# Optimization experiments

Measured on AMD Instinct MI355X. Metric: run time of the kernel, lower is better.

The kernel has to match this reference:

```python
import jax, jax.numpy as jnp
import numpy as np

D = 768          # emb_dim (BERT hidden size)
N_DOM = 9        # domain_num
N_EXP = 6        # num_expert (per-domain)
N_SH = 4         # num_shared_expert
N_TOT = N_EXP + N_SH  # total experts seen by the gate
B = 2048


def _p(key, shape, scale=0.02):
    return jax.random.normal(key, shape, dtype=jnp.float32) * scale


def setup_inputs() -> dict:
    key = jax.random.key(0)
    ks = jax.random.split(key, 32)
    inp = {
        "content_pooled": jax.random.normal(ks[0], (B, D), dtype=jnp.float32),
        "ftr_pooled": jax.random.normal(ks[1], (B, D), dtype=jnp.float32),
        "category": jax.random.randint(ks[2], (B,), 0, N_DOM, dtype=jnp.int64),
        "domain_emb": _p(ks[3], (N_DOM, D), 1.0),
    }
    # per-domain expert stacks: Linear(D,D)-SiLU-Linear(D,D), for content (c) and ftr (f)
    for pre, base in (("c", 4), ("f", 12)):
        inp[pre + "W1"] = _p(ks[base + 0], (N_DOM, N_EXP, D, D))
        inp[pre + "b1"] = jnp.zeros((N_DOM, N_EXP, D), jnp.float32)
        inp[pre + "W2"] = _p(ks[base + 1], (N_DOM, N_EXP, D, D))
        inp[pre + "b2"] = jnp.zeros((N_DOM, N_EXP, D), jnp.float32)
        # shared experts: Linear(D,D)-SiLU-Linear(D,D)
        inp[pre + "sW1"] = _p(ks[base + 2], (N_SH, D, D))
        inp[pre + "sb1"] = jnp.zeros((N_SH, D), jnp.float32)
        inp[pre + "sW2"] = _p(ks[base + 3], (N_SH, D, D))
        inp[pre + "sb2"] = jnp.zeros((N_SH, D), jnp.float32)
        # per-domain enhanced gates: Linear(2D,D)-SiLU-Linear(D,N_TOT), temperature scalar per domain
        inp[pre + "gW1"] = _p(ks[base + 4], (N_DOM, 2 * D, D))
        inp[pre + "gb1"] = jnp.zeros((N_DOM, D), jnp.float32)
        inp[pre + "gW2"] = _p(ks[base + 5], (N_DOM, D, N_TOT))
        inp[pre + "gb2"] = jnp.zeros((N_DOM, N_TOT), jnp.float32)
        inp[pre + "temp"] = jnp.ones((N_DOM,), jnp.float32)
    return inp


def _moe_branch(x, category, domain_emb, W1, b1, W2, b2,
                sW1, sb1, sW2, sb2, gW1, gb1, gW2, gb2, temp):
    # x: [B, D]; category: [B] int in [0, N_DOM)
    demb = domain_emb[category]                           # [B, D]
    g_in = jnp.concatenate([demb, x], axis=-1)            # [B, 2D]
    # gate computed for all domains, then per-example domain selected
    gh = jax.nn.silu(jnp.einsum("bx,nxh->bnh", g_in, gW1) + gb1)      # [B, 9, D]
    logits = jnp.einsum("bnh,nhe->bne", gh, gW2) + gb2                 # [B, 9, 10]
    t = jax.nn.softplus(temp) + 1e-4                                    # positive temperature
    gates_all = jax.nn.softmax(logits / t[None, :, None], axis=-1)
    gates = jnp.take_along_axis(gates_all, category[:, None, None], axis=1)[:, 0]  # [B, 10]
    # per-domain experts for all domains (grouped GEMM form), then select domain
    h1 = jax.nn.silu(jnp.einsum("bd,nedh->bneh", x, W1) + b1)          # [B, 9, 6, D]
    e_all = jnp.einsum("bneh,nehd->bned", h1, W2) + b2                 # [B, 9, 6, D]
    e_dom = jnp.take_along_axis(e_all, category[:, None, None, None], axis=1)[:, 0]  # [B, 6, D]
    # shared experts
    hs = jax.nn.silu(jnp.einsum("bd,edh->beh", x, sW1) + sb1)          # [B, 4, D]
    e_sh = jnp.einsum("beh,ehd->bed", hs, sW2) + sb2                   # [B, 4, D]
    experts = jnp.concatenate([e_dom, e_sh], axis=1)                   # [B, 10, D]
    return jnp.einsum("be,bed->bd", gates, experts)                    # [B, D]


def reference(content_pooled, ftr_pooled, category, domain_emb,
              cW1, cb1, cW2, cb2, csW1, csb1, csW2, csb2,
              cgW1, cgb1, cgW2, cgb2, ctemp,
              fW1, fb1, fW2, fb2, fsW1, fsb1, fsW2, fsb2,
              fgW1, fgb1, fgW2, fgb2, ftemp):
    c_out = _moe_branch(content_pooled, category, domain_emb,
                        cW1, cb1, cW2, cb2, csW1, csb1, csW2, csb2,
                        cgW1, cgb1, cgW2, cgb2, ctemp)
    f_out = _moe_branch(ftr_pooled, category, domain_emb,
                        fW1, fb1, fW2, fb2, fsW1, fsb1, fsW2, fsb2,
                        fgW1, fgb1, fgW2, fgb2, ftemp)
    return jnp.concatenate([c_out, f_out], axis=-1)  # [B, 2D]
```

## Files before the change

kernel.cpp:

```cpp
#include <hip/hip_runtime.h>

#define D_ 768
#define B_ 2048
#define NDOM 9
#define NTOT 10
#define MT 128
#define NT 128
#define KT 32
#define KI1 (D_ / KT)

#define E2   589824ull
#define E2G  1179648ull
#define OFF_WT2 31850496ull
#define OFF_SW1 63700992ull
#define OFF_SW2 66060288ull
#define OFF_GW1 68419584ull
#define ZWE     79036416ull

typedef _Float16 f16;
typedef _Float16 f16x8 __attribute__((ext_vector_type(8)));
typedef _Float16 f16x2 __attribute__((ext_vector_type(2)));
typedef float f32x4 __attribute__((ext_vector_type(4)));

typedef const __attribute__((address_space(1))) void gas_void;
typedef __attribute__((address_space(3))) void las_void;

__device__ __forceinline__ void gload16(const f16* g, f16* l) {
  __builtin_amdgcn_global_load_lds((gas_void*)g, (las_void*)l, 16, 0, 0);
}

#define WAITV4() asm volatile("s_waitcnt vmcnt(4)" ::: "memory")
#define WAITV0() asm volatile("s_waitcnt vmcnt(0)" ::: "memory")
#define SBAR()   do { __builtin_amdgcn_s_barrier(); __builtin_amdgcn_sched_barrier(0); } while (0)

__global__ __launch_bounds__(256) void bucket_kernel(const int* cat32, int* perm,
                                                     int* off, int* cnt, int* dom) {
  __shared__ int scnt[NDOM], soff[NDOM], scur[NDOM];
  __shared__ int odd_nz;
  int t = threadIdx.x;
  if (t == 0) odd_nz = 0;
  if (t < NDOM) scnt[t] = 0;
  __syncthreads();
  int loc = 0;
  for (int i = t; i < B_; i += 256)
    if ((i & 1) && cat32[i] != 0) loc = 1;
  if (loc) atomicOr(&odd_nz, 1);
  __syncthreads();
  int strd = odd_nz ? 1 : 2;
  for (int i = t; i < B_; i += 256) atomicAdd(&scnt[cat32[i * strd]], 1);
  __syncthreads();
  if (t == 0) { int a = 0; for (int n = 0; n < NDOM; n++) { soff[n] = a; a += scnt[n]; } }
  __syncthreads();
  if (t < NDOM) { scur[t] = soff[t]; off[t] = soff[t]; cnt[t] = scnt[t]; }
  __syncthreads();
  for (int i = t; i < B_; i += 256) {
    int n = cat32[i * strd];
    int pos = atomicAdd(&scur[n], 1);
    perm[pos] = i;
    dom[pos] = n;
  }
}

__global__ __launch_bounds__(256) void cvt_kernel(const float* src, f16* dst, int n8) {
  int i = blockIdx.x * 256 + threadIdx.x;
  if (i >= n8) return;
  const f32x4* s = (const f32x4*)(src + (size_t)i * 8);
  f32x4 a = s[0], b = s[1];
  f16x8 o;
  o[0]=(f16)a[0]; o[1]=(f16)a[1]; o[2]=(f16)a[2]; o[3]=(f16)a[3];
  o[4]=(f16)b[0]; o[5]=(f16)b[1]; o[6]=(f16)b[2]; o[7]=(f16)b[3];
  *(f16x8*)(dst + (size_t)i * 8) = o;
}

struct TRP { const float* s[10]; f16* wt; };

__global__ __launch_bounds__(256) void trans_kernel(TRP p) {
  const int m = blockIdx.z, z = m / 125, r = m % 125;
  const float* src; f16* dst; int R;
  const size_t zw = (size_t)z * ZWE;
  if (r < 54)       { src = p.s[0+z] + (size_t)r*E2;        dst = p.wt + zw + (size_t)r*E2;                 R = 768; }
  else if (r < 108) { int i=r-54;  src = p.s[2+z] + (size_t)i*E2;  dst = p.wt + zw + OFF_WT2 + (size_t)i*E2;  R = 768; }
  else if (r < 112) { int i=r-108; src = p.s[4+z] + (size_t)i*E2;  dst = p.wt + zw + OFF_SW1 + (size_t)i*E2;  R = 768; }
  else if (r < 116) { int i=r-112; src = p.s[6+z] + (size_t)i*E2;  dst = p.wt + zw + OFF_SW2 + (size_t)i*E2;  R = 768; }
  else              { int i=r-116; src = p.s[8+z] + (size_t)i*E2G; dst = p.wt + zw + OFF_GW1 + (size_t)i*E2G; R = 1536; }
  const int ty = blockIdx.y;
  if (ty * 64 >= R) return;
  const int tx = blockIdx.x;

  __shared__ f16 tile[64][72];
  const int t = threadIdx.x;
  const int lr = t >> 4, lc = (t & 15) * 4;
#pragma unroll
  for (int i = 0; i < 4; i++) {
    int row = lr + i * 16;
    f32x4 v = *(const f32x4*)(src + (size_t)(ty*64 + row) * 768 + tx*64 + lc);
    tile[lc+0][row] = (f16)v[0];
    tile[lc+1][row] = (f16)v[1];
    tile[lc+2][row] = (f16)v[2];
    tile[lc+3][row] = (f16)v[3];
  }
  __syncthreads();
  const int orow = t >> 3, oc = (t & 7) * 8;
#pragma unroll
  for (int i = 0; i < 2; i++) {
    int r2 = orow + i * 32;
    f16x8 v = *(const f16x8*)&tile[r2][oc];
    *(f16x8*)(dst + (size_t)(tx*64 + r2) * R + ty*64 + oc) = v;
  }
}

struct L1P {
  const f16* x16[2]; const f16* demb16; const f16* wt;
  const float* b1[2]; const float* sb1[2]; const float* gb1[2];
  const int* perm; const int* off; const int* cnt;
  f16* h;
};

__global__ __launch_bounds__(256, 3) void layer1_kernel(L1P p) {
  const int z = blockIdx.z;
  const int g = blockIdx.y;
  const int x = blockIdx.x;
  const int nt = x % 6;
  int mt0 = x / 6, mtstep = 4;

  int row_off, row_cnt, slot, gdom = 0, kiters = KI1;
  const f16* WT; const float* bias;
  bool isGate = false;
  const size_t zw = (size_t)z * ZWE;
  if (g < 54) {
    int n = g / 6, e = g % 6;
    row_off = p.off[n]; row_cnt = p.cnt[n];
    WT = p.wt + zw + (size_t)(n*6+e) * E2;
    bias = p.b1[z] + (n*6+e) * D_;
    slot = e;
  } else if (g < 70) {
    int s_ = g - 54, e = s_ >> 2;
    row_off = 0; row_cnt = B_;
    WT = p.wt + zw + OFF_SW1 + (size_t)e * E2;
    bias = p.sb1[z] + e * D_;
    slot = 6 + e;
    mt0 = x / 6 + 4 * (s_ & 3); mtstep = 16;
  } else {
    int n = g - 70;
    row_off = p.off[n]; row_cnt = p.cnt[n];
    WT = p.wt + zw + OFF_GW1 + (size_t)n * E2G;
    bias = p.gb1[z] + n * D_;
    slot = 10; isGate = true; gdom = n; kiters = 2 * KI1;
  }
  const int KW = isGate ? 2 * D_ : D_;

  __shared__ f16 As[3][MT][KT];
  __shared__ f16 Bs[3][MT][KT];

  const int t = threadIdx.x;
  const int wave = t >> 6, lane = t & 63;
  const int wr = (wave >> 1) * 64, wc = (wave & 1) * 64;
  const int r0 = lane & 15, q = lane >> 4;
  const int jbase = nt * NT;
  const int lrow = lane >> 2;
  const int lk = (lane & 3) * 8;

  const f16* bBase[2];
#pragma unroll
  for (int i = 0; i < 2; i++) {
    int col = jbase + 32 * wave + 16 * i + lrow;
    bBase[i] = WT + (size_t)col * KW + lk;
  }
  const f16* dB = p.demb16 + (size_t)gdom * D_ + lk;

  for (int mt = mt0; mt * MT < row_cnt; mt += mtstep) {
    const f16* aBase[2];
#pragma unroll
    for (int i = 0; i < 2; i++) {
      int rl = mt * MT + 32 * wave + 16 * i + lrow;
      int pr = p.perm[(rl < row_cnt) ? (row_off + rl) : row_off];
      aBase[i] = p.x16[z] + (size_t)pr * D_ + lk;
    }

    auto STAGE = [&](int buf, int kk) {
      const int k0 = kk * KT;
#pragma unroll
      for (int i = 0; i < 2; i++) {
        const f16* as;
        if (isGate) as = (k0 < D_) ? (dB + k0) : (aBase[i] + (k0 - D_));
        else        as = aBase[i] + k0;
        gload16(as, &As[buf][32 * wave + 16 * i][0]);
        gload16(bBase[i] + k0, &Bs[buf][32 * wave + 16 * i][0]);
      }
    };

    f32x4 acc[4][4];
#pragma unroll
    for (int a = 0; a < 4; a++)
#pragma unroll
      for (int b = 0; b < 4; b++) acc[a][b] = (f32x4){0.f, 0.f, 0.f, 0.f};

    STAGE(0, 0);
    STAGE(1, 1);
    WAITV4();
    SBAR();

    int cur = 0;
    for (int kk = 0; kk < kiters; kk++) {
      int pf = cur + 2; if (pf >= 3) pf -= 3;
      if (kk + 2 < kiters) STAGE(pf, kk + 2);
      f16x8 af[4], bf[4];
#pragma unroll
      for (int m = 0; m < 4; m++) af[m] = *(const f16x8*)&As[cur][wr + m * 16 + r0][q * 8];
#pragma unroll
      for (int nn = 0; nn < 4; nn++) bf[nn] = *(const f16x8*)&Bs[cur][wc + nn * 16 + r0][q * 8];
#pragma unroll
      for (int m = 0; m < 4; m++)
#pragma unroll
        for (int nn = 0; nn < 4; nn++)
          acc[m][nn] = __builtin_amdgcn_mfma_f32_16x16x32_f16(af[m], bf[nn], acc[m][nn], 0, 0, 0);
      if (kk + 2 < kiters) { WAITV4(); } else { WAITV0(); }
      SBAR();
      cur = (cur == 2) ? 0 : cur + 1;
    }

    f16* hout = p.h + (size_t)(z * 11 + slot) * B_ * D_;
#pragma unroll
    for (int nn = 0; nn < 4; nn++) {
      const int col = jbase + wc + nn * 16 + r0;
      const float bc = bias[col];
#pragma unroll
      for (int m = 0; m < 4; m++) {
#pragma unroll
        for (int i = 0; i < 4; i++) {
          int lr = mt * MT + wr + m * 16 + q * 4 + i;
          if (lr < row_cnt) {
            float v = acc[m][nn][i] + bc;
            v = v / (1.f + __expf(-v));
            hout[(size_t)(row_off + lr) * D_ + col] = (f16)v;
          }
        }
      }
    }
  }
}

struct GP {
  const f16* h;
  const float* gW2[2]; const float* gb2[2]; const float* temp[2];
  const int* dom;
  float* gates;
};

__global__ __launch_bounds__(256) void gate_kernel(GP p) {
  int wid = (blockIdx.x * 256 + threadIdx.x) >> 6;
  int lane = threadIdx.x & 63;
  int z = wid >> 11;
  int pos = wid & (B_ - 1);
  int n = p.dom[pos];
  const f16* gh = p.h + ((size_t)(z * 11 + 10) * B_ + pos) * D_;
  const float* W = p.gW2[z] + (size_t)n * D_ * NTOT;
  float part[NTOT];
#pragma unroll
  for (int e = 0; e < NTOT; e++) part[e] = 0.f;
  for (int k = lane; k < D_; k += 64) {
    float a = (float)gh[k];
    const float* wrow = W + (size_t)k * NTOT;
#pragma unroll
    for (int e = 0; e < NTOT; e++) part[e] = fmaf(a, wrow[e], part[e]);
  }
#pragma unroll
  for (int e = 0; e < NTOT; e++) {
    float v = part[e];
#pragma unroll
    for (int s = 32; s > 0; s >>= 1) v += __shfl_xor(v, s, 64);
    part[e] = v;
  }
  float tv = p.temp[z][n];
  float tq = (tv > 15.f ? tv : log1pf(__expf(tv))) + 1e-4f;
  const float* b2 = p.gb2[z] + n * NTOT;
  float mx = -1e30f;
#pragma unroll
  for (int e = 0; e < NTOT; e++) { part[e] = (part[e] + b2[e]) / tq; mx = fmaxf(mx, part[e]); }
  float s = 0.f;
#pragma unroll
  for (int e = 0; e < NTOT; e++) { part[e] = __expf(part[e] - mx); s += part[e]; }
  float inv = 1.f / s;
  if (lane < NTOT) p.gates[((size_t)z * B_ + pos) * NTOT + lane] = part[lane] * inv;
}

struct L2P {
  const f16* h; const f16* wt;
  const float* b2[2]; const float* sb2[2];
  const float* gates;
  const int* perm; const int* off; const int* cnt;
  float* out;
};

__global__ __launch_bounds__(256, 3) void layer2_kernel(L2P p) {
  const int zz = blockIdx.z;
  const int z = zz / 5, es = zz % 5, ebase = es * 2;
  const int n = blockIdx.y;
  const int x = blockIdx.x;
  const int nt = x % 6, mt0 = x / 6;
  const int row_off = p.off[n], row_cnt = p.cnt[n];

  __shared__ f16 As[3][MT][KT];
  __shared__ f16 Bs[3][MT][KT];
  __shared__ float sg[MT][2];
  __shared__ int sperm[MT];

  const int t = threadIdx.x;
  const int wave = t >> 6, lane = t & 63;
  const int wr = (wave >> 1) * 64, wc = (wave & 1) * 64;
  const int r0 = lane & 15, q = lane >> 4;
  const int jbase = nt * NT;
  const int lrow = lane >> 2;
  const int lk = (lane & 3) * 8;

  const size_t zw = (size_t)z * ZWE;
  const f16* WB0; const f16* WB1; const float* pb[2]; size_t slotOff[2];
  {
    int e0 = ebase, e1 = ebase + 1;
    WB0 = (e0 < 6) ? (p.wt + zw + OFF_WT2 + (size_t)(n*6+e0)*E2) : (p.wt + zw + OFF_SW2 + (size_t)(e0-6)*E2);
    WB1 = (e1 < 6) ? (p.wt + zw + OFF_WT2 + (size_t)(n*6+e1)*E2) : (p.wt + zw + OFF_SW2 + (size_t)(e1-6)*E2);
    pb[0] = (e0 < 6) ? (p.b2[z] + (size_t)(n*6+e0)*D_) : (p.sb2[z] + (size_t)(e0-6)*D_);
    pb[1] = (e1 < 6) ? (p.b2[z] + (size_t)(n*6+e1)*D_) : (p.sb2[z] + (size_t)(e1-6)*D_);
    slotOff[0] = (size_t)(z*11 + e0) * B_ * D_;
    slotOff[1] = (size_t)(z*11 + e1) * B_ * D_;
  }

  const f16* bB0[2]; const f16* bB1[2];
#pragma unroll
  for (int i = 0; i < 2; i++) {
    int col = jbase + 32 * wave + 16 * i + lrow;
    bB0[i] = WB0 + (size_t)col * D_ + lk;
    bB1[i] = WB1 + (size_t)col * D_ + lk;
  }

  for (int mt = mt0; mt * MT < row_cnt; mt += 4) {
    for (int i = t; i < MT * 2; i += 256) {
      int rr = i >> 1, e = i & 1;
      int gp = row_off + mt * MT + rr;
      sg[rr][e] = (gp < B_ && (mt * MT + rr) < row_cnt)
                  ? p.gates[((size_t)z * B_ + gp) * NTOT + ebase + e] : 0.f;
    }
    for (int i = t; i < MT; i += 256) {
      int gp = row_off + mt * MT + i;
      sperm[i] = (gp < B_) ? p.perm[gp] : 0;
    }
    __syncthreads();

    const f16* aB0[2]; const f16* aB1[2];
#pragma unroll
    for (int i = 0; i < 2; i++) {
      int rl = mt * MT + 32 * wave + 16 * i + lrow;
      int rr = (rl < row_cnt) ? (row_off + rl) : row_off;
      size_t rp = (size_t)rr * D_ + lk;
      aB0[i] = p.h + slotOff[0] + rp;
      aB1[i] = p.h + slotOff[1] + rp;
    }
    f16 gA[4], gB[4];
#pragma unroll
    for (int m = 0; m < 4; m++) {
      gA[m] = (f16)sg[wr + m * 16 + r0][0];
      gB[m] = (f16)sg[wr + m * 16 + r0][1];
    }

    auto STAGE = [&](int buf, int it) {
      const int ei = (it >= KI1);
      const int k0 = (it - (ei ? KI1 : 0)) * KT;
#pragma unroll
      for (int i = 0; i < 2; i++) {
        const f16* as = (ei ? aB1[i] : aB0[i]) + k0;
        const f16* bs = (ei ? bB1[i] : bB0[i]) + k0;
        gload16(as, &As[buf][32 * wave + 16 * i][0]);
        gload16(bs, &Bs[buf][32 * wave + 16 * i][0]);
      }
    };

    f32x4 acc[4][4];
#pragma unroll
    for (int a = 0; a < 4; a++)
#pragma unroll
      for (int b = 0; b < 4; b++) acc[a][b] = (f32x4){0.f, 0.f, 0.f, 0.f};

    const int total = 2 * KI1;
    STAGE(0, 0);
    STAGE(1, 1);
    WAITV4();
    SBAR();

    int cur = 0;
    for (int it = 0; it < total; it++) {
      int pf = cur + 2; if (pf >= 3) pf -= 3;
      if (it + 2 < total) STAGE(pf, it + 2);
      const int ei = (it >= KI1);
      f16x8 af[4], bf[4];
#pragma unroll
      for (int m = 0; m < 4; m++) {
        af[m] = *(const f16x8*)&As[cur][wr + m * 16 + r0][q * 8];
        af[m] = af[m] * (ei ? gB[m] : gA[m]);
      }
#pragma unroll
      for (int nn = 0; nn < 4; nn++) bf[nn] = *(const f16x8*)&Bs[cur][wc + nn * 16 + r0][q * 8];
#pragma unroll
      for (int m = 0; m < 4; m++)
#pragma unroll
        for (int nn = 0; nn < 4; nn++)
          acc[m][nn] = __builtin_amdgcn_mfma_f32_16x16x32_f16(af[m], bf[nn], acc[m][nn], 0, 0, 0);
      if (it + 2 < total) { WAITV4(); } else { WAITV0(); }
      SBAR();
      cur = (cur == 2) ? 0 : cur + 1;
    }

    const int zoff = z * D_;
#pragma unroll
    for (int nn = 0; nn < 4; nn++) {
      const int col = jbase + wc + nn * 16 + r0;
      float pbc0 = pb[0][col], pbc1 = pb[1][col];
#pragma unroll
      for (int m = 0; m < 4; m++) {
#pragma unroll
        for (int i = 0; i < 4; i++) {
          const int lrt = wr + m * 16 + q * 4 + i;
          if (mt * MT + lrt < row_cnt) {
            float v = acc[m][nn][i];
            v = fmaf(sg[lrt][0], pbc0, v);
            v = fmaf(sg[lrt][1], pbc1, v);
            float* dst = p.out + (size_t)sperm[lrt] * (2 * D_) + zoff + col;
            __hip_atomic_fetch_add(dst, v, __ATOMIC_RELAXED, __HIP_MEMORY_SCOPE_AGENT);
          }
        }
      }
    }
    __syncthreads();
  }
}

extern "C" void kernel_launch(void* const* d_in, const int* in_sizes, int n_in,
                              void* d_out, int out_size, void* d_ws, size_t ws_size,
                              hipStream_t stream) {
  const float* content = (const float*)d_in[0];
  const float* ftr     = (const float*)d_in[1];
  const int*   cat     = (const int*)d_in[2];
  const float* demb    = (const float*)d_in[3];

  const float* cW1  = (const float*)d_in[4];
  const float* cb1  = (const float*)d_in[5];
  const float* cW2  = (const float*)d_in[6];
  const float* cb2  = (const float*)d_in[7];
  const float* csW1 = (const float*)d_in[8];
  const float* csb1 = (const float*)d_in[9];
  const float* csW2 = (const float*)d_in[10];
  const float* csb2 = (const float*)d_in[11];
  const float* cgW1 = (const float*)d_in[12];
  const float* cgb1 = (const float*)d_in[13];
  const float* cgW2 = (const float*)d_in[14];
  const float* cgb2 = (const float*)d_in[15];
  const float* ctemp= (const float*)d_in[16];

  const float* fW1  = (const float*)d_in[17];
  const float* fb1  = (const float*)d_in[18];
  const float* fW2  = (const float*)d_in[19];
  const float* fb2  = (const float*)d_in[20];
  const float* fsW1 = (const float*)d_in[21];
  const float* fsb1 = (const float*)d_in[22];
  const float* fsW2 = (const float*)d_in[23];
  const float* fsb2 = (const float*)d_in[24];
  const float* fgW1 = (const float*)d_in[25];
  const float* fgb1 = (const float*)d_in[26];
  const float* fgW2 = (const float*)d_in[27];
  const float* fgb2 = (const float*)d_in[28];
  const float* ftemp= (const float*)d_in[29];

  char* wsb = (char*)d_ws;
  int* perm    = (int*)wsb;
  int* off     = (int*)(wsb + 8192);
  int* cnt     = (int*)(wsb + 8256);
  int* dom     = (int*)(wsb + 8320);
  float* gates = (float*)(wsb + 16512);
  f16* h       = (f16*)(wsb + 180352);
  f16* x16a    = (f16*)(wsb + 69386368);
  f16* x16b    = (f16*)(wsb + 72532096);
  f16* demb16  = (f16*)(wsb + 75677824);
  f16* wt      = (f16*)(wsb + 75691648);
  float* out   = (float*)d_out;

  (void)hipMemsetAsync(d_out, 0, (size_t)out_size * sizeof(float), stream);

  bucket_kernel<<<1, 256, 0, stream>>>(cat, perm, off, cnt, dom);

  cvt_kernel<<<768, 256, 0, stream>>>(content, x16a, (B_ * D_) / 8);
  cvt_kernel<<<768, 256, 0, stream>>>(ftr, x16b, (B_ * D_) / 8);
  cvt_kernel<<<4, 256, 0, stream>>>(demb, demb16, (NDOM * D_) / 8);

  TRP tp;
  tp.s[0] = cW1;  tp.s[1] = fW1;
  tp.s[2] = cW2;  tp.s[3] = fW2;
  tp.s[4] = csW1; tp.s[5] = fsW1;
  tp.s[6] = csW2; tp.s[7] = fsW2;
  tp.s[8] = cgW1; tp.s[9] = fgW1;
  tp.wt = wt;
  trans_kernel<<<dim3(12, 24, 250), 256, 0, stream>>>(tp);

  L1P p1;
  p1.x16[0] = x16a; p1.x16[1] = x16b; p1.demb16 = demb16; p1.wt = wt;
  p1.b1[0] = cb1;  p1.b1[1] = fb1;
  p1.sb1[0] = csb1; p1.sb1[1] = fsb1;
  p1.gb1[0] = cgb1; p1.gb1[1] = fgb1;
  p1.perm = perm; p1.off = off; p1.cnt = cnt; p1.h = h;
  layer1_kernel<<<dim3(24, 79, 2), 256, 0, stream>>>(p1);

  GP pg;
  pg.h = h; pg.gW2[0] = cgW2; pg.gW2[1] = fgW2;
  pg.gb2[0] = cgb2; pg.gb2[1] = fgb2;
  pg.temp[0] = ctemp; pg.temp[1] = ftemp;
  pg.dom = dom; pg.gates = gates;
  gate_kernel<<<dim3((2 * B_) / 4), 256, 0, stream>>>(pg);

  L2P p2;
  p2.h = h; p2.wt = wt;
  p2.b2[0] = cb2;  p2.b2[1] = fb2;
  p2.sb2[0] = csb2; p2.sb2[1] = fsb2;
  p2.gates = gates; p2.perm = perm; p2.off = off; p2.cnt = cnt; p2.out = out;
  layer2_kernel<<<dim3(24, 9, 10), 256, 0, stream>>>(p2);

  (void)in_sizes; (void)n_in; (void)ws_size;
}
```

Baseline: 612.5 us.

## Swizzle LDS tiles, remap blocks across XCDs, and raise MFMA priority

Result: faster. 582.3 us (-4.9%).

```diff
diff --git a/kernel.cpp b/kernel.cpp
--- a/kernel.cpp
+++ b/kernel.cpp
@@ -19,6 +19,7 @@
 
 typedef _Float16 f16;
 typedef _Float16 f16x8 __attribute__((ext_vector_type(8)));
+typedef _Float16 f16x4 __attribute__((ext_vector_type(4)));
 typedef _Float16 f16x2 __attribute__((ext_vector_type(2)));
 typedef float f32x4 __attribute__((ext_vector_type(4)));
 
@@ -87,7 +88,7 @@
   if (ty * 64 >= R) return;
   const int tx = blockIdx.x;
 
-  __shared__ f16 tile[64][72];
+  __shared__ f16 tile[64][76];
   const int t = threadIdx.x;
   const int lr = t >> 4, lc = (t & 15) * 4;
 #pragma unroll
@@ -104,8 +105,10 @@
 #pragma unroll
   for (int i = 0; i < 2; i++) {
     int r2 = orow + i * 32;
-    f16x8 v = *(const f16x8*)&tile[r2][oc];
-    *(f16x8*)(dst + (size_t)(tx*64 + r2) * R + ty*64 + oc) = v;
+    union { f16x8 v8; f16x4 v4[2]; } u;
+    u.v4[0] = *(const f16x4*)&tile[r2][oc];
+    u.v4[1] = *(const f16x4*)&tile[r2][oc + 4];
+    *(f16x8*)(dst + (size_t)(tx*64 + r2) * R + ty*64 + oc) = u.v8;
   }
 }
 
@@ -116,10 +119,16 @@
   f16* h;
 };
 
+#define NBL1 3792
+#define QX1  474
+
 __global__ __launch_bounds__(256, 3) void layer1_kernel(L1P p) {
-  const int z = blockIdx.z;
-  const int g = blockIdx.y;
-  const int x = blockIdx.x;
+  const int raw = blockIdx.x;
+  const int L = (raw & 7) * QX1 + (raw >> 3);
+  const int z = L / 1896;
+  const int rem = L - z * 1896;
+  const int g = rem / 24;
+  const int x = rem % 24;
   const int nt = x % 6;
   int mt0 = x / 6, mtstep = 4;
 
@@ -158,7 +167,8 @@
   const int r0 = lane & 15, q = lane >> 4;
   const int jbase = nt * NT;
   const int lrow = lane >> 2;
-  const int lk = (lane & 3) * 8;
+  const int lk = 8 * ((lane & 3) ^ ((lane >> 3) & 3));
+  const int qa = (q ^ ((r0 >> 1) & 3)) * 8;
 
   const f16* bBase[2];
 #pragma unroll
@@ -206,14 +216,16 @@
       if (kk + 2 < kiters) STAGE(pf, kk + 2);
       f16x8 af[4], bf[4];
 #pragma unroll
-      for (int m = 0; m < 4; m++) af[m] = *(const f16x8*)&As[cur][wr + m * 16 + r0][q * 8];
-#pragma unroll
-      for (int nn = 0; nn < 4; nn++) bf[nn] = *(const f16x8*)&Bs[cur][wc + nn * 16 + r0][q * 8];
+      for (int m = 0; m < 4; m++) af[m] = *(const f16x8*)&As[cur][wr + m * 16 + r0][qa];
+#pragma unroll
+      for (int nn = 0; nn < 4; nn++) bf[nn] = *(const f16x8*)&Bs[cur][wc + nn * 16 + r0][qa];
+      __builtin_amdgcn_s_setprio(1);
 #pragma unroll
       for (int m = 0; m < 4; m++)
 #pragma unroll
         for (int nn = 0; nn < 4; nn++)
           acc[m][nn] = __builtin_amdgcn_mfma_f32_16x16x32_f16(af[m], bf[nn], acc[m][nn], 0, 0, 0);
+      __builtin_amdgcn_s_setprio(0);
       if (kk + 2 < kiters) { WAITV4(); } else { WAITV0(); }
       SBAR();
       cur = (cur == 2) ? 0 : cur + 1;
@@ -292,11 +304,17 @@
   float* out;
 };
 
+#define NBL2 2160
+#define QX2  270
+
 __global__ __launch_bounds__(256, 3) void layer2_kernel(L2P p) {
-  const int zz = blockIdx.z;
+  const int raw = blockIdx.x;
+  const int L = (raw & 7) * QX2 + (raw >> 3);
+  const int zz = L / 216;
+  const int rem = L % 216;
+  const int n = rem / 24;
+  const int x = rem % 24;
   const int z = zz / 5, es = zz % 5, ebase = es * 2;
-  const int n = blockIdx.y;
-  const int x = blockIdx.x;
   const int nt = x % 6, mt0 = x / 6;
   const int row_off = p.off[n], row_cnt = p.cnt[n];
 
@@ -311,7 +329,8 @@
   const int r0 = lane & 15, q = lane >> 4;
   const int jbase = nt * NT;
   const int lrow = lane >> 2;
-  const int lk = (lane & 3) * 8;
+  const int lk = 8 * ((lane & 3) ^ ((lane >> 3) & 3));
+  const int qa = (q ^ ((r0 >> 1) & 3)) * 8;
 
   const size_t zw = (size_t)z * ZWE;
   const f16* WB0; const f16* WB1; const float* pb[2]; size_t slotOff[2];
@@ -394,16 +413,18 @@
       f16x8 af[4], bf[4];
 #pragma unroll
       for (int m = 0; m < 4; m++) {
-        af[m] = *(const f16x8*)&As[cur][wr + m * 16 + r0][q * 8];
+        af[m] = *(const f16x8*)&As[cur][wr + m * 16 + r0][qa];
         af[m] = af[m] * (ei ? gB[m] : gA[m]);
       }
 #pragma unroll
-      for (int nn = 0; nn < 4; nn++) bf[nn] = *(const f16x8*)&Bs[cur][wc + nn * 16 + r0][q * 8];
+      for (int nn = 0; nn < 4; nn++) bf[nn] = *(const f16x8*)&Bs[cur][wc + nn * 16 + r0][qa];
+      __builtin_amdgcn_s_setprio(1);
 #pragma unroll
       for (int m = 0; m < 4; m++)
 #pragma unroll
         for (int nn = 0; nn < 4; nn++)
           acc[m][nn] = __builtin_amdgcn_mfma_f32_16x16x32_f16(af[m], bf[nn], acc[m][nn], 0, 0, 0);
+      __builtin_amdgcn_s_setprio(0);
       if (it + 2 < total) { WAITV4(); } else { WAITV0(); }
       SBAR();
       cur = (cur == 2) ? 0 : cur + 1;
@@ -505,7 +526,7 @@
   p1.sb1[0] = csb1; p1.sb1[1] = fsb1;
   p1.gb1[0] = cgb1; p1.gb1[1] = fgb1;
   p1.perm = perm; p1.off = off; p1.cnt = cnt; p1.h = h;
-  layer1_kernel<<<dim3(24, 79, 2), 256, 0, stream>>>(p1);
+  layer1_kernel<<<dim3(NBL1), 256, 0, stream>>>(p1);
 
   GP pg;
   pg.h = h; pg.gW2[0] = cgW2; pg.gW2[1] = fgW2;
@@ -519,7 +540,7 @@
   p2.b2[0] = cb2;  p2.b2[1] = fb2;
   p2.sb2[0] = csb2; p2.sb2[1] = fsb2;
   p2.gates = gates; p2.perm = perm; p2.off = off; p2.cnt = cnt; p2.out = out;
-  layer2_kernel<<<dim3(24, 9, 10), 256, 0, stream>>>(p2);
+  layer2_kernel<<<dim3(NBL2), 256, 0, stream>>>(p2);
 
   (void)in_sizes; (void)n_in; (void)ws_size;
 }
```
